# Optimization experiments

Measured on AMD Instinct MI355X. Metric: run time of the kernel, lower is better.

## Reference

```python
import jax, jax.numpy as jnp
import numpy as np

B, D = 65536, 1024
E = 10   # experts per group (shared and per-task)
H = 10   # expert hidden units
T = 2    # tasks
G = 20   # gate units = task experts + shared experts


def setup_inputs() -> dict:
    key = jax.random.key(0)
    ks = jax.random.split(key, 8)
    s = 1.0 / np.sqrt(D)
    return {
        "x": jax.random.normal(ks[0], (B, D), dtype=jnp.float32),
        "show_index": jax.random.randint(ks[1], (B,), 0, 100, dtype=jnp.int64),
        "st": jax.random.normal(ks[2], (B, 8), dtype=jnp.float32),
        "Ws": jax.random.normal(ks[3], (E, D, H), dtype=jnp.float32) * s,
        "bs": jnp.zeros((E, H), dtype=jnp.float32),
        "Wt": jax.random.normal(ks[4], (T, E, D, H), dtype=jnp.float32) * s,
        "bt": jnp.zeros((T, E, H), dtype=jnp.float32),
        "Wg": jax.random.normal(ks[5], (T, D, G), dtype=jnp.float32) * s,
        "bg": jnp.zeros((T, G), dtype=jnp.float32),
        "Wc": jax.random.normal(ks[6], (H, 1), dtype=jnp.float32),
        "bc": jnp.zeros((1,), dtype=jnp.float32),
        "Wv": jax.random.normal(ks[7], (H, 1), dtype=jnp.float32),
        "bv": jnp.zeros((1,), dtype=jnp.float32),
    }


def reference(x, show_index, st, Ws, bs, Wt, bt, Wg, bg, Wc, bc, Wv, bv):
    # shared experts: [B, H, E]  (Dense(H,relu) per expert, stacked on axis 2)
    share = jax.nn.relu(jnp.einsum('bd,edh->bhe', x, Ws) + bs.T)

    def task_tower(i):
        gate = jax.nn.softmax(x @ Wg[i] + bg[i], axis=-1)               # [B, G]
        task = jax.nn.relu(jnp.einsum('bd,edh->bhe', x, Wt[i]) + bt[i].T)  # [B, H, E]
        merge = jnp.concatenate([task, share], axis=2)                  # [B, H, G]
        # gate broadcast over H (repeat_elements on axis 1), sum over experts
        return jnp.sum(merge * gate[:, None, :], axis=2)                # [B, H]

    f0 = task_tower(0)
    f1 = task_tower(1)
    ctr_logits = jax.nn.sigmoid(f0 @ Wc + bc)  # [B, 1]
    cvr_logits = jax.nn.sigmoid(f1 @ Wv + bv)  # [B, 1]
    return (ctr_logits, cvr_logits)
```

## Files before the change

### kernel.cpp

```cpp
#include <hip/hip_runtime.h>
#include <hip/hip_bf16.h>

typedef __attribute__((ext_vector_type(8))) short bf16x8;
typedef __attribute__((ext_vector_type(4))) float f32x4;

#define NCOLP 384
#define STEP_SHORTS (NCOLP * 32)
#define STEP_BYTES 24576
#define SEG_BYTES 6144
#define NSTEP 32
#define BROWS 65536
#define QSZ 32768

static __device__ __forceinline__ unsigned int bf16rne(float f) {
  unsigned int u = __float_as_uint(f);
  return (u + 0x7FFFu + ((u >> 16) & 1u)) >> 16;
}
static __device__ __forceinline__ unsigned int pack2(float a, float b) {
  return bf16rne(a) | (bf16rne(b) << 16);
}

__global__ void ple_prep(const float* __restrict__ Ws, const float* __restrict__ bs,
                         const float* __restrict__ Wt, const float* __restrict__ bt,
                         const float* __restrict__ Wg, const float* __restrict__ bg,
                         unsigned short* __restrict__ Wpack, float* __restrict__ bias) {
  const int n = blockIdx.x;
  const int tid = threadIdx.x;
  const float* src = nullptr;
  int stride = 0;
  float bval = 0.f;
  if (n < 200) {
    int t = n / 100, m = n % 100, e = m / 10, h = m % 10;
    src = Wt + (size_t)(t * 10 + e) * 10240 + h;
    stride = 10;
    bval = bt[(t * 10 + e) * 10 + h];
  } else if (n < 300) {
    int m = n - 200, e = m / 10, h = m % 10;
    src = Ws + (size_t)e * 10240 + h;
    stride = 10;
    bval = bs[e * 10 + h];
  } else if (n < 340) {
    int m = n - 300, t = m / 20, g = m % 20;
    src = Wg + (size_t)t * 20480 + g;
    stride = 20;
    bval = bg[t * 20 + g];
  }
  for (int j = 0; j < 4; j++) {
    int k = tid + j * 256;
    float v = src ? src[(size_t)k * stride] : 0.f;
    Wpack[(size_t)(k >> 5) * STEP_SHORTS + ((k >> 3) & 3) * (NCOLP * 8) + n * 8 +
          (k & 7)] = (unsigned short)bf16rne(v);
  }
  if (tid == 0 && n < 352) bias[n] = bval;
}

__global__ __launch_bounds__(256, 2) void ple_main(
    const float* __restrict__ x, const unsigned short* __restrict__ Wpack,
    const float* __restrict__ bias, const float* __restrict__ Wc,
    const float* __restrict__ bc, const float* __restrict__ Wv,
    const float* __restrict__ bv, float* __restrict__ out) {
  __shared__ __align__(16) char smem[2 * QSZ];
  float* z = (float*)smem;

  const int tid = threadIdx.x;
  const int l = tid & 63, w = tid >> 6;
  const int arow = l & 15, ablk = l >> 4;
  const int rowbase = blockIdx.x * 64;
  const int q0 = (int)(blockIdx.x & 3);

  const f32x4 fzero = {0.f, 0.f, 0.f, 0.f};
  f32x4 acc[4][6];
#pragma unroll
  for (int i = 0; i < 4; ++i)
#pragma unroll
    for (int j = 0; j < 6; ++j) acc[i][j] = fzero;

  const char* bbase = (const char*)Wpack + ablk * SEG_BYTES +
                      (w * 96 + arow) * 16;
  bf16x8 b0[6], b1[6], b2[6];

  const char* xstage = (const char*)x + (size_t)(rowbase + w) * 4096 + l * 16;
  float4 g[8], hgrp[8];

#define GISSUE(P, G, J0)                                                       \
  {                                                                            \
    const int qp = (q0 + (P)) & 3;                                             \
    _Pragma("unroll") for (int j = 0; j < 8; j++)                              \
        G[j] = *(const float4*)(xstage + (size_t)((J0) + j) * 4 * 4096 +       \
                                qp * 1024);                                    \
  }
#define GWRITE(P, G, J0)                                                       \
  {                                                                            \
    _Pragma("unroll") for (int j = 0; j < 8; j++) {                            \
      const int row = w + ((J0) + j) * 4;                                      \
      const int s = l >> 1;                                                    \
      const int segp = (s & 24) | ((s & 7) ^ (row & 7));                       \
      uint2 u;                                                                 \
      u.x = pack2(G[j].x, G[j].y);                                             \
      u.y = pack2(G[j].z, G[j].w);                                             \
      *(uint2*)(smem + ((P)&1) * QSZ + row * 512 + segp * 16 + (l & 1) * 8) =  \
          u;                                                                   \
    }                                                                          \
  }
#define STEPX(I, BU, BP)                                                       \
  {                                                                            \
    const int ipre = ((I) + 2 <= 31) ? (I) + 2 : 31;                           \
    const int kpre = (q0 * 8 + ipre) & 31;                                     \
    const char* bp = bbase + (size_t)kpre * STEP_BYTES;                        \
    _Pragma("unroll") for (int nt = 0; nt < 6; nt++)                           \
        BP[nt] = *(const bf16x8*)(bp + nt * 256);                              \
    _Pragma("unroll") for (int mf = 0; mf < 4; mf++) {                         \
      const int s = ((I)&7) * 4 + ablk;                                        \
      const int segp = (s & 24) | ((s & 7) ^ (arow & 7));                      \
      const bf16x8 av =                                                        \
          *(const bf16x8*)(smem + (((I) >> 3) & 1) * QSZ +                     \
                           (mf * 16 + arow) * 512 + segp * 16);                \
      _Pragma("unroll") for (int nt = 0; nt < 6; nt++)                         \
          acc[mf][nt] = __builtin_amdgcn_mfma_f32_16x16x32_bf16(               \
              av, BU[nt], acc[mf][nt], 0, 0, 0);                               \
    }                                                                          \
  }
#define SB __builtin_amdgcn_sched_barrier(0);
#define QBAR                                                                   \
  asm volatile("s_waitcnt lgkmcnt(0)" ::: "memory");                           \
  __builtin_amdgcn_s_barrier();

#pragma unroll
  for (int nt = 0; nt < 6; nt++) {
    b0[nt] = *(const bf16x8*)(bbase + (size_t)((q0 * 8) & 31) * STEP_BYTES +
                              nt * 256);
    b1[nt] = *(const bf16x8*)(bbase +
                              (size_t)((q0 * 8 + 1) & 31) * STEP_BYTES +
                              nt * 256);
  }
  SB
  GISSUE(0, g, 0) SB GWRITE(0, g, 0) SB GISSUE(0, hgrp, 8) SB
  GWRITE(0, hgrp, 8) QBAR SB

  STEPX(0, b0, b2) STEPX(1, b1, b0)
  SB GISSUE(1, g, 0) SB
  STEPX(2, b2, b1) STEPX(3, b0, b2) STEPX(4, b1, b0)
  SB GWRITE(1, g, 0) SB GISSUE(1, hgrp, 8) SB
  STEPX(5, b2, b1) STEPX(6, b0, b2) STEPX(7, b1, b0)
  SB GWRITE(1, hgrp, 8) QBAR SB

  STEPX(8, b2, b1) STEPX(9, b0, b2)
  SB GISSUE(2, g, 0) SB
  STEPX(10, b1, b0) STEPX(11, b2, b1) STEPX(12, b0, b2)
  SB GWRITE(2, g, 0) SB GISSUE(2, hgrp, 8) SB
  STEPX(13, b1, b0) STEPX(14, b2, b1) STEPX(15, b0, b2)
  SB GWRITE(2, hgrp, 8) QBAR SB

  STEPX(16, b1, b0) STEPX(17, b2, b1)
  SB GISSUE(3, g, 0) SB
  STEPX(18, b0, b2) STEPX(19, b1, b0) STEPX(20, b2, b1)
  SB GWRITE(3, g, 0) SB GISSUE(3, hgrp, 8) SB
  STEPX(21, b0, b2) STEPX(22, b1, b0) STEPX(23, b2, b1)
  SB GWRITE(3, hgrp, 8) QBAR SB

  STEPX(24, b0, b2) STEPX(25, b1, b0) STEPX(26, b2, b1) STEPX(27, b0, b2)
  STEPX(28, b1, b0) STEPX(29, b2, b1) STEPX(30, b0, b2) STEPX(31, b1, b0)
  QBAR

#undef QBAR
#undef SB
#undef STEPX
#undef GWRITE
#undef GISSUE

#pragma unroll
  for (int p = 0; p < 2; p++) {
    __syncthreads();
#pragma unroll
    for (int q = 0; q < 2; q++) {
      const int mf = p * 2 + q;
#pragma unroll
      for (int nt = 0; nt < 6; nt++) {
        if (w == 3 && nt >= 4) continue;
#pragma unroll
        for (int r = 0; r < 4; r++)
          z[(q * 16 + ablk * 4 + r) * 357 + w * 96 + nt * 16 + arow] =
              acc[mf][nt][r];
      }
    }
    __syncthreads();
    {
      const int item = tid >> 2, sub = tid & 3;
      const int t = item >> 5, r = item & 31;
      const float* zr = &z[r * 357];
      float gl[5], m = -1e30f;
#pragma unroll
      for (int v = 0; v < 5; v++) {
        const int u = sub * 5 + v;
        gl[v] = zr[300 + t * 20 + u] + bias[300 + t * 20 + u];
        m = fmaxf(m, gl[v]);
      }
      m = fmaxf(m, __shfl_xor(m, 1));
      m = fmaxf(m, __shfl_xor(m, 2));
      const float* Wl = t ? Wv : Wc;
      float wl[10];
#pragma unroll
      for (int h = 0; h < 10; h++) wl[h] = Wl[h];
      float s = 0.f, accum = 0.f;
#pragma unroll
      for (int v = 0; v < 5; v++) {
        const int u = sub * 5 + v;
        const float pu = __expf(gl[v] - m);
        s += pu;
        const int cbase = (u < 10) ? (t * 100 + u * 10) : (200 + (u - 10) * 10);
        float d = 0.f;
#pragma unroll
        for (int h = 0; h < 10; h++)
          d += fmaxf(zr[cbase + h] + bias[cbase + h], 0.f) * wl[h];
        accum += pu * d;
      }
      s += __shfl_xor(s, 1);
      s += __shfl_xor(s, 2);
      accum += __shfl_xor(accum, 1);
      accum += __shfl_xor(accum, 2);
      if (sub == 0) {
        const float logit = (t ? bv[0] : bc[0]) + accum / s;
        out[(size_t)t * BROWS + rowbase + p * 32 + r] =
            1.f / (1.f + __expf(-logit));
      }
    }
  }
}

extern "C" void kernel_launch(void* const* d_in, const int* in_sizes, int n_in,
                              void* d_out, int out_size, void* d_ws, size_t ws_size,
                              hipStream_t stream) {
  const float* x = (const float*)d_in[0];
  const float* Ws = (const float*)d_in[3];
  const float* bs = (const float*)d_in[4];
  const float* Wt = (const float*)d_in[5];
  const float* bt = (const float*)d_in[6];
  const float* Wg = (const float*)d_in[7];
  const float* bg = (const float*)d_in[8];
  const float* Wc = (const float*)d_in[9];
  const float* bc = (const float*)d_in[10];
  const float* Wv = (const float*)d_in[11];
  const float* bv = (const float*)d_in[12];
  unsigned short* Wpack = (unsigned short*)d_ws;
  float* bias = (float*)((char*)d_ws + (size_t)NCOLP * 1024 * 2);
  float* out = (float*)d_out;

  hipLaunchKernelGGL(ple_prep, dim3(NCOLP), dim3(256), 0, stream, Ws, bs, Wt, bt,
                     Wg, bg, Wpack, bias);
  hipLaunchKernelGGL(ple_main, dim3(BROWS / 64), dim3(256), 0, stream, x, Wpack,
                     bias, Wc, bc, Wv, bv, out);
}
```

Measured before the change: 78.00 us.

## Stage x tiles via direct global-to-LDS loads in fp32 and convert on read

Replaces the register-staged load, bf16 pack and LDS write of x quarter-tiles with async global_load_lds transfers that put raw fp32 data straight into a doubled 128KB LDS buffer. The bf16 conversion moves to the A-fragment read inside each MFMA step. Each step now issues its slice of the next quarter's loads, with vmcnt-based waits before barriers. The goal is to cut VGPR staging and VALU work in the load path and overlap it with the MFMAs. In exchange, LDS use and LDS read traffic double, the pack work is repeated for every read, and occupancy drops to one block per CU.

Measured after the change: 139.5 us. +78.8%, slower.

```diff
diff --git a/kernel.cpp b/kernel.cpp
--- a/kernel.cpp
+++ b/kernel.cpp
@@ -10,7 +10,7 @@
 #define SEG_BYTES 6144
 #define NSTEP 32
 #define BROWS 65536
-#define QSZ 32768
+#define QSZF 65536
 
 static __device__ __forceinline__ unsigned int bf16rne(float f) {
   unsigned int u = __float_as_uint(f);
@@ -18,6 +18,11 @@
 }
 static __device__ __forceinline__ unsigned int pack2(float a, float b) {
   return bf16rne(a) | (bf16rne(b) << 16);
+}
+static __device__ __forceinline__ void gload16(const void* g, void* l) {
+  __builtin_amdgcn_global_load_lds(
+      (const __attribute__((address_space(1))) unsigned int*)g,
+      (__attribute__((address_space(3))) unsigned int*)l, 16, 0, 0);
 }
 
 __global__ void ple_prep(const float* __restrict__ Ws, const float* __restrict__ bs,
@@ -54,12 +59,12 @@
   if (tid == 0 && n < 352) bias[n] = bval;
 }
 
-__global__ __launch_bounds__(256, 2) void ple_main(
+__global__ __launch_bounds__(256, 1) void ple_main(
     const float* __restrict__ x, const unsigned short* __restrict__ Wpack,
     const float* __restrict__ bias, const float* __restrict__ Wc,
     const float* __restrict__ bc, const float* __restrict__ Wv,
     const float* __restrict__ bv, float* __restrict__ out) {
-  __shared__ __align__(16) char smem[2 * QSZ];
+  __shared__ __align__(16) char smem[2 * QSZF];
   float* z = (float*)smem;
 
   const int tid = threadIdx.x;
@@ -79,28 +84,20 @@
                       (w * 96 + arow) * 16;
   bf16x8 b0[6], b1[6], b2[6];
 
-  const char* xstage = (const char*)x + (size_t)(rowbase + w) * 4096 + l * 16;
-  float4 g[8], hgrp[8];
-
-#define GISSUE(P, G, J0)                                                       \
+  const char* srcE = (const char*)x + (size_t)(rowbase + w) * 4096 +
+                     (((l >> 1) ^ w) * 32) + ((l & 1) * 16);
+  const char* srcO = (const char*)x + (size_t)(rowbase + w) * 4096 +
+                     (((l >> 1) ^ (w + 4)) * 32) + ((l & 1) * 16);
+  char* dstb = smem + tid * 16;
+
+#define GL2(PPOS, J)                                                           \
   {                                                                            \
-    const int qp = (q0 + (P)) & 3;                                             \
-    _Pragma("unroll") for (int j = 0; j < 8; j++)                              \
-        G[j] = *(const float4*)(xstage + (size_t)((J0) + j) * 4 * 4096 +       \
-                                qp * 1024);                                    \
-  }
-#define GWRITE(P, G, J0)                                                       \
-  {                                                                            \
-    _Pragma("unroll") for (int j = 0; j < 8; j++) {                            \
-      const int row = w + ((J0) + j) * 4;                                      \
-      const int s = l >> 1;                                                    \
-      const int segp = (s & 24) | ((s & 7) ^ (row & 7));                       \
-      uint2 u;                                                                 \
-      u.x = pack2(G[j].x, G[j].y);                                             \
-      u.y = pack2(G[j].z, G[j].w);                                             \
-      *(uint2*)(smem + ((P)&1) * QSZ + row * 512 + segp * 16 + (l & 1) * 8) =  \
-          u;                                                                   \
-    }                                                                          \
+    const int qp = (q0 + (PPOS)) & 3;                                          \
+    const size_t so = (size_t)((PPOS)&1) * QSZF;                               \
+    gload16(srcE + (size_t)(8 * (J)) * 4096 + qp * 1024,                       \
+            dstb + so + (size_t)(2 * (J)) * 4096);                             \
+    gload16(srcO + (size_t)(8 * (J) + 4) * 4096 + qp * 1024,                   \
+            dstb + so + (size_t)(2 * (J) + 1) * 4096);                         \
   }
 #define STEPX(I, BU, BP)                                                       \
   {                                                                            \
@@ -110,21 +107,27 @@
     _Pragma("unroll") for (int nt = 0; nt < 6; nt++)                           \
         BP[nt] = *(const bf16x8*)(bp + nt * 256);                              \
     _Pragma("unroll") for (int mf = 0; mf < 4; mf++) {                         \
-      const int s = ((I)&7) * 4 + ablk;                                        \
-      const int segp = (s & 24) | ((s & 7) ^ (arow & 7));                      \
-      const bf16x8 av =                                                        \
-          *(const bf16x8*)(smem + (((I) >> 3) & 1) * QSZ +                     \
-                           (mf * 16 + arow) * 512 + segp * 16);                \
+      const int phys = (((I)&7) * 4 + ablk) ^ (arow & 7);                      \
+      const char* ar = smem + (size_t)(((I) >> 3) & 1) * QSZF +                \
+                       (mf * 16 + arow) * 1024 + phys * 32;                    \
+      const float4 fa = *(const float4*)(ar);                                  \
+      const float4 fb = *(const float4*)(ar + 16);                             \
+      union { bf16x8 v; uint4 u; } A;                                          \
+      A.u = make_uint4(pack2(fa.x, fa.y), pack2(fa.z, fa.w),                   \
+                       pack2(fb.x, fb.y), pack2(fb.z, fb.w));                  \
       _Pragma("unroll") for (int nt = 0; nt < 6; nt++)                         \
           acc[mf][nt] = __builtin_amdgcn_mfma_f32_16x16x32_bf16(               \
-              av, BU[nt], acc[mf][nt], 0, 0, 0);                               \
+              A.v, BU[nt], acc[mf][nt], 0, 0, 0);                              \
     }                                                                          \
   }
 #define SB __builtin_amdgcn_sched_barrier(0);
-#define QBAR                                                                   \
-  asm volatile("s_waitcnt lgkmcnt(0)" ::: "memory");                           \
+#define QBAR6                                                                  \
+  asm volatile("s_waitcnt vmcnt(6)" ::: "memory");                             \
   __builtin_amdgcn_s_barrier();
 
+  GL2(0, 0) GL2(0, 1) GL2(0, 2) GL2(0, 3)
+  GL2(0, 4) GL2(0, 5) GL2(0, 6) GL2(0, 7)
+  SB
 #pragma unroll
   for (int nt = 0; nt < 6; nt++) {
     b0[nt] = *(const bf16x8*)(bbase + (size_t)((q0 * 8) & 31) * STEP_BYTES +
@@ -134,39 +137,48 @@
                               nt * 256);
   }
   SB
-  GISSUE(0, g, 0) SB GWRITE(0, g, 0) SB GISSUE(0, hgrp, 8) SB
-  GWRITE(0, hgrp, 8) QBAR SB
-
-  STEPX(0, b0, b2) STEPX(1, b1, b0)
-  SB GISSUE(1, g, 0) SB
-  STEPX(2, b2, b1) STEPX(3, b0, b2) STEPX(4, b1, b0)
-  SB GWRITE(1, g, 0) SB GISSUE(1, hgrp, 8) SB
-  STEPX(5, b2, b1) STEPX(6, b0, b2) STEPX(7, b1, b0)
-  SB GWRITE(1, hgrp, 8) QBAR SB
-
-  STEPX(8, b2, b1) STEPX(9, b0, b2)
-  SB GISSUE(2, g, 0) SB
-  STEPX(10, b1, b0) STEPX(11, b2, b1) STEPX(12, b0, b2)
-  SB GWRITE(2, g, 0) SB GISSUE(2, hgrp, 8) SB
-  STEPX(13, b1, b0) STEPX(14, b2, b1) STEPX(15, b0, b2)
-  SB GWRITE(2, hgrp, 8) QBAR SB
-
-  STEPX(16, b1, b0) STEPX(17, b2, b1)
-  SB GISSUE(3, g, 0) SB
-  STEPX(18, b0, b2) STEPX(19, b1, b0) STEPX(20, b2, b1)
-  SB GWRITE(3, g, 0) SB GISSUE(3, hgrp, 8) SB
-  STEPX(21, b0, b2) STEPX(22, b1, b0) STEPX(23, b2, b1)
-  SB GWRITE(3, hgrp, 8) QBAR SB
+  asm volatile("s_waitcnt vmcnt(12)" ::: "memory");
+  __builtin_amdgcn_s_barrier();
+  SB
+
+  GL2(1, 0) SB STEPX(0, b0, b2) SB
+  GL2(1, 1) SB STEPX(1, b1, b0) SB
+  GL2(1, 2) SB STEPX(2, b2, b1) SB
+  GL2(1, 3) SB STEPX(3, b0, b2) SB
+  GL2(1, 4) SB STEPX(4, b1, b0) SB
+  GL2(1, 5) SB STEPX(5, b2, b1) SB
+  GL2(1, 6) SB STEPX(6, b0, b2) SB
+  GL2(1, 7) SB STEPX(7, b1, b0) SB
+  QBAR6 SB
+
+  GL2(2, 0) SB STEPX(8, b2, b1) SB
+  GL2(2, 1) SB STEPX(9, b0, b2) SB
+  GL2(2, 2) SB STEPX(10, b1, b0) SB
+  GL2(2, 3) SB STEPX(11, b2, b1) SB
+  GL2(2, 4) SB STEPX(12, b0, b2) SB
+  GL2(2, 5) SB STEPX(13, b1, b0) SB
+  GL2(2, 6) SB STEPX(14, b2, b1) SB
+  GL2(2, 7) SB STEPX(15, b0, b2) SB
+  QBAR6 SB
+
+  GL2(3, 0) SB STEPX(16, b1, b0) SB
+  GL2(3, 1) SB STEPX(17, b2, b1) SB
+  GL2(3, 2) SB STEPX(18, b0, b2) SB
+  GL2(3, 3) SB STEPX(19, b1, b0) SB
+  GL2(3, 4) SB STEPX(20, b2, b1) SB
+  GL2(3, 5) SB STEPX(21, b0, b2) SB
+  GL2(3, 6) SB STEPX(22, b1, b0) SB
+  GL2(3, 7) SB STEPX(23, b2, b1) SB
+  QBAR6 SB
 
   STEPX(24, b0, b2) STEPX(25, b1, b0) STEPX(26, b2, b1) STEPX(27, b0, b2)
   STEPX(28, b1, b0) STEPX(29, b2, b1) STEPX(30, b0, b2) STEPX(31, b1, b0)
-  QBAR
-
-#undef QBAR
+
+#undef QBAR6
 #undef SB
 #undef STEPX
-#undef GWRITE
-#undef GISSUE
+#undef GL2
+  __syncthreads();
 
 #pragma unroll
   for (int p = 0; p < 2; p++) {
```
